# Performance work log

Measured on AMD Instinct MI355X. Metric: run time of the kernel, lower is better.

## Reference

```python
import jax, jax.numpy as jnp
import numpy as np

HQ, HK, DH = 32, 8, 64
ROPE_BASE = 10000.0


def _rope_tables(T, dtype):
    pos = jnp.arange(T, dtype=jnp.float32)
    inv_freq = 1.0 / (ROPE_BASE ** (jnp.arange(0, DH, 2, dtype=jnp.float32) / DH))
    freqs = pos[:, None] * inv_freq[None, :]          # (T, DH/2)
    cos = jnp.concatenate([jnp.cos(freqs), jnp.cos(freqs)], -1).astype(dtype)  # (T, DH)
    sin = jnp.concatenate([jnp.sin(freqs), jnp.sin(freqs)], -1).astype(dtype)
    return cos, sin


def _rotate_half(t):
    return jnp.concatenate([-t[..., DH // 2:], t[..., :DH // 2]], -1)


def setup_inputs() -> dict:
    key = jax.random.key(0)
    k1, k2, k3, k4 = jax.random.split(key, 4)
    B, T, D = 2, 2048, 2048
    std = 0.02 / np.sqrt(24)
    kv_std = std / np.sqrt(HQ / HK)
    return {
        "x": jax.random.normal(k1, (B, T, D), jnp.float32),
        "Wq": jax.random.normal(k2, (D, HQ * DH), jnp.float32) * std,
        "Wkv": jax.random.normal(k3, (D, 2 * HK * DH), jnp.float32) * kv_std,
        "Wo": jax.random.normal(k4, (HQ * DH, D), jnp.float32) * std,
    }


def reference(x, Wq, Wkv, Wo):
    B, T, D = x.shape
    g = HQ // HK
    scale = DH ** -0.5
    # projections
    q = (x @ Wq).reshape(B, T, HQ, DH).transpose(0, 2, 1, 3)       # (B,Hq,T,Dh)
    kv = (x @ Wkv).reshape(B, T, 2, HK, DH)
    k = kv[:, :, 0].transpose(0, 2, 1, 3)                           # (B,Hk,T,Dh)
    v = kv[:, :, 1].transpose(0, 2, 1, 3)
    # GQA expand: each kv head repeated g times consecutively
    k = jnp.repeat(k, g, axis=1)                                    # (B,Hq,T,Dh)
    v = jnp.repeat(v, g, axis=1)
    # RoPE on q and repeated k
    cos, sin = _rope_tables(T, x.dtype)
    q = q * cos + _rotate_half(q) * sin
    k = k * cos + _rotate_half(k) * sin
    # attention
    scores = jnp.einsum('bhqd,bhkd->bhqk', q, k) * scale            # (B,Hq,T,T)
    causal = jnp.triu(jnp.ones((T, T), bool), 1)
    scores = jnp.where(causal, -jnp.inf, scores)
    attn = jax.nn.softmax(scores.astype(jnp.float32), axis=-1).astype(x.dtype)
    out = jnp.einsum('bhqk,bhkd->bhqd', attn, v)                    # (B,Hq,T,Dh)
    out = out.transpose(0, 2, 1, 3).reshape(B, T, HQ * DH)
    return out @ Wo
```

## Files before the change

### kernel.cpp

```cpp
#include <hip/hip_runtime.h>
#include <hip/hip_bf16.h>

#define DEVI __device__ __forceinline__

typedef __attribute__((ext_vector_type(4))) float f32x4;
typedef __attribute__((ext_vector_type(16))) float f32x16;
typedef __attribute__((ext_vector_type(8))) short s16x8;
typedef __attribute__((ext_vector_type(4))) short s16x4;

DEVI ushort f2bf(float f) {
  union { float f; unsigned u; } v; v.f = f;
  unsigned r = v.u + 0x7FFFu + ((v.u >> 16) & 1u);
  return (ushort)(r >> 16);
}

DEVI void gload_lds16(const void* g, void* l) {
  __builtin_amdgcn_global_load_lds((const __attribute__((address_space(1))) void*)g,
                                   (__attribute__((address_space(3))) void*)l, 16, 0, 0);
}

template <int NITER>
DEVI void stage_swz(const ushort* __restrict__ gsrc, int stride_elems, ushort* lds, int tid) {
  const int wv = tid >> 6, ln = tid & 63;
  #pragma unroll
  for (int j = 0; j < NITER; ++j) {
    const int ci = j * 256 + wv * 64 + ln;
    const int row = ci >> 3, c = ci & 7;
    const ushort* src = gsrc + (size_t)row * stride_elems + ((c ^ (row & 7)) << 3);
    gload_lds16(src, lds + (size_t)(j * 256 + wv * 64) * 8);
  }
}

DEVI s16x8 frag_swz(const ushort* lds_tile, int row, int chunk) {
  const int off = row * 128 + ((chunk ^ (row & 7)) << 4);
  return *(const s16x8*)((const char*)lds_tile + off);
}

__global__ __launch_bounds__(256) void cast_bf16_k(const float* __restrict__ in,
                                                   ushort* __restrict__ out, int n) {
  int i = (blockIdx.x * 256 + threadIdx.x) * 4;
  if (i >= n) return;
  float4 v = *(const float4*)(in + i);
  ushort4 o;
  o.x = f2bf(v.x); o.y = f2bf(v.y); o.z = f2bf(v.z); o.w = f2bf(v.w);
  *(ushort4*)(out + i) = o;
}

__global__ __launch_bounds__(256) void transpose_cast_k(const float* __restrict__ in,
                                                        ushort* __restrict__ out, int R, int C) {
  __shared__ ushort tile[64][66];
  const int r0 = blockIdx.y * 64, c0 = blockIdx.x * 64;
  const int tid = threadIdx.x;
  #pragma unroll
  for (int j = 0; j < 16; ++j) {
    int idx = j * 256 + tid;
    int r = idx >> 6, c = idx & 63;
    tile[c][r] = f2bf(in[(size_t)(r0 + r) * C + c0 + c]);
  }
  __syncthreads();
  #pragma unroll
  for (int j = 0; j < 16; ++j) {
    int idx = j * 256 + tid;
    int c = idx >> 6, r = idx & 63;
    out[(size_t)(c0 + c) * R + r0 + r] = tile[c][r];
  }
}

__global__ __launch_bounds__(256) void rope_table_k(float2* __restrict__ tab) {
  int idx = blockIdx.x * 256 + threadIdx.x;
  int t = idx >> 5, i = idx & 31;
  float inv = expf(-(float)i * 0.28782313662425575f);
  float ang = (float)t * inv;
  tab[idx] = make_float2(cosf(ang), sinf(ang));
}

__global__ __launch_bounds__(256) void gemm_bt(const ushort* __restrict__ A,
                                               const ushort* __restrict__ BT,
                                               float* __restrict__ C, int M, int N, int K) {
  __shared__ __align__(128) ushort As[128 * 64];
  __shared__ __align__(128) ushort Bs[128 * 64];
  const int tid = threadIdx.x;
  const int ln = tid & 63, wv = tid >> 6;
  const int g = ln >> 4, l15 = ln & 15;
  const int wm = wv >> 1, wn = wv & 1;
  const int m0 = blockIdx.y * 128, n0 = blockIdx.x * 128;

  f32x4 zero = {0.f, 0.f, 0.f, 0.f};
  f32x4 acc[4][4];
  #pragma unroll
  for (int i = 0; i < 4; ++i)
    #pragma unroll
    for (int j = 0; j < 4; ++j) acc[i][j] = zero;

  for (int kt = 0; kt < K; kt += 64) {
    __syncthreads();
    stage_swz<4>(A + (size_t)m0 * K + kt, K, As, tid);
    stage_swz<4>(BT + (size_t)n0 * K + kt, K, Bs, tid);
    __syncthreads();
    #pragma unroll
    for (int ks = 0; ks < 2; ++ks) {
      s16x8 af[4], bfr[4];
      #pragma unroll
      for (int mi = 0; mi < 4; ++mi) af[mi] = frag_swz(As, wm * 64 + mi * 16 + l15, ks * 4 + g);
      #pragma unroll
      for (int ni = 0; ni < 4; ++ni) bfr[ni] = frag_swz(Bs, wn * 64 + ni * 16 + l15, ks * 4 + g);
      #pragma unroll
      for (int mi = 0; mi < 4; ++mi)
        #pragma unroll
        for (int ni = 0; ni < 4; ++ni)
          acc[mi][ni] = __builtin_amdgcn_mfma_f32_16x16x32_bf16(af[mi], bfr[ni], acc[mi][ni], 0, 0, 0);
    }
  }
  #pragma unroll
  for (int mi = 0; mi < 4; ++mi)
    #pragma unroll
    for (int r = 0; r < 4; ++r) {
      int row = m0 + wm * 64 + mi * 16 + g * 4 + r;
      float* crow = C + (size_t)row * N + n0 + wn * 64 + l15;
      #pragma unroll
      for (int ni = 0; ni < 4; ++ni) crow[ni * 16] = acc[mi][ni][r];
    }
}

__global__ __launch_bounds__(256) void gemm_qkv_fused(const ushort* __restrict__ A,
                                                      const ushort* __restrict__ BT,
                                                      const float2* __restrict__ tab,
                                                      ushort* __restrict__ Qp,
                                                      ushort* __restrict__ Kp,
                                                      ushort* __restrict__ Vp) {
  const int K = 2048;
  __shared__ __align__(128) ushort smem[128 * 132];
  ushort* As = smem;
  ushort* Bs = smem + 8192;
  ushort* Ot = smem;
  const int tid = threadIdx.x;
  const int ln = tid & 63, wv = tid >> 6;
  const int g = ln >> 4, l15 = ln & 15;
  const int l31 = ln & 31, hi = ln >> 5;
  const int wm = wv >> 1, wn = wv & 1;
  const int m0 = blockIdx.y * 128, n0 = blockIdx.x * 128;

  f32x4 zero = {0.f, 0.f, 0.f, 0.f};
  f32x4 acc[4][4];
  #pragma unroll
  for (int i = 0; i < 4; ++i)
    #pragma unroll
    for (int j = 0; j < 4; ++j) acc[i][j] = zero;

  for (int kt = 0; kt < K; kt += 64) {
    __syncthreads();
    stage_swz<4>(A + (size_t)m0 * K + kt, K, As, tid);
    stage_swz<4>(BT + (size_t)n0 * K + kt, K, Bs, tid);
    __syncthreads();
    #pragma unroll
    for (int ks = 0; ks < 2; ++ks) {
      s16x8 af[4], bfr[4];
      #pragma unroll
      for (int mi = 0; mi < 4; ++mi) af[mi] = frag_swz(As, wm * 64 + mi * 16 + l15, ks * 4 + g);
      #pragma unroll
      for (int ni = 0; ni < 4; ++ni) bfr[ni] = frag_swz(Bs, wn * 64 + ni * 16 + l15, ks * 4 + g);
      #pragma unroll
      for (int mi = 0; mi < 4; ++mi)
        #pragma unroll
        for (int ni = 0; ni < 4; ++ni)
          acc[mi][ni] = __builtin_amdgcn_mfma_f32_16x16x32_bf16(af[mi], bfr[ni], acc[mi][ni], 0, 0, 0);
    }
  }

  __syncthreads();
  const int bq = m0 >> 11;
  const int tg0 = m0 & 2047;
  const int type = (n0 < 2048) ? 0 : (n0 < 2560 ? 1 : 2);

  #pragma unroll
  for (int mi = 0; mi < 4; ++mi)
    #pragma unroll
    for (int r = 0; r < 4; ++r) {
      const int tl = wm * 64 + mi * 16 + g * 4 + r;
      const int t = tg0 + tl;
      #pragma unroll
      for (int ni = 0; ni < 4; ++ni) {
        const int cl = wn * 64 + ni * 16 + l15;
        float val = acc[mi][ni][r];
        float outv;
        if (type < 2) {
          float pairv = acc[mi][ni ^ 2][r];
          float2 cs = tab[t * 32 + (ni & 1) * 16 + l15];
          outv = (ni & 2) ? (val * cs.x + pairv * cs.y) : (val * cs.x - pairv * cs.y);
          if (type == 0) outv *= 0.18033688011112042f;
        } else {
          outv = val;
        }
        Ot[tl * 132 + cl] = f2bf(outv);
      }
    }
  __syncthreads();

  #pragma unroll
  for (int it = 0; it < 8; ++it) {
    const int id = wv * 8 + it;
    const int hl = id >> 4, q4 = (id >> 2) & 3, fi = id & 3;
    const int tile = (tg0 >> 5) + q4;
    if (type < 2) {
      const ushort* srow = Ot + (q4 * 32 + l31) * 132 + hl * 64 + fi * 16 + hi * 8;
      union { s16x4 h[2]; s16x8 v; } u;
      u.h[0] = *(const s16x4*)srow;
      u.h[1] = *(const s16x4*)(srow + 4);
      ushort* dst;
      if (type == 0) {
        const int h = (n0 >> 6) + hl;
        dst = Qp + (((size_t)(bq * 32 + h) * 64 + tile) * 4 + fi) * 512 + ln * 8;
      } else {
        const int h = ((n0 - 2048) >> 6) + hl;
        dst = Kp + (((size_t)(bq * 8 + h) * 64 + tile) * 4 + fi) * 512 + ln * 8;
      }
      *(s16x8*)dst = u.v;
    } else {
      const int hk = ((n0 - 2560) >> 6) + hl;
      const int col = hl * 64 + (fi & 1) * 32 + l31;
      const int row0 = q4 * 32 + (fi >> 1) * 16 + hi * 8;
      ushort o[8];
      #pragma unroll
      for (int j = 0; j < 8; ++j) o[j] = Ot[(row0 + j) * 132 + col];
      ushort* dst = Vp + (((size_t)(bq * 8 + hk) * 64 + tile) * 4 + fi) * 512 + ln * 8;
      *(s16x8*)dst = *(const s16x8*)o;
    }
  }
}

__global__ __launch_bounds__(256) void attn_k(const ushort* __restrict__ Qp,
                                              const ushort* __restrict__ Kp,
                                              const ushort* __restrict__ Vp,
                                              ushort* __restrict__ O) {
  __shared__ ushort ep[4][32 * 64];
  const int tid = threadIdx.x, wv = tid >> 6, ln = tid & 63;
  const int l31 = ln & 31, hi = ln >> 5;

  const int f = blockIdx.x + gridDim.x * (blockIdx.y + 32 * blockIdx.z);
  const int xcd = f & 7, j = f >> 3;
  const int pr = xcd + 8 * (j & 1);
  const int b = pr >> 3, hk = pr & 7;
  const int s = j >> 1;
  const int hq = hk * 4 + (s & 3);
  const int qtile = 63 - ((s >> 2) * 4 + wv);
  const int qw = qtile * 32;
  const int nt = qtile + 1;

  const ushort* Qh    = Qp + ((size_t)(b * 32 + hq)) * (64 * 2048);
  const ushort* Kbase = Kp + ((size_t)(b * 8 + hk)) * (64 * 2048);
  const ushort* Vbase = Vp + ((size_t)(b * 8 + hk)) * (64 * 2048);
  ushort* lds = ep[wv];

  s16x8 qf[4];
  {
    const ushort* qp_ = Qh + (size_t)qtile * 2048 + ln * 8;
    #pragma unroll
    for (int ks = 0; ks < 4; ++ks) qf[ks] = *(const s16x8*)(qp_ + ks * 512);
  }

  f32x16 oacc[2];
  #pragma unroll
  for (int dt = 0; dt < 2; ++dt)
    #pragma unroll
    for (int r = 0; r < 16; ++r) oacc[dt][r] = 0.f;
  float m = -1e30f, l = 0.f;

  const ushort* kp = Kbase + ln * 8;
  const ushort* vp = Vbase + ln * 8;

  s16x8 kf[4];
  #pragma unroll
  for (int ks = 0; ks < 4; ++ks) kf[ks] = *(const s16x8*)(kp + ks * 512);
  kp += 2048;

  s16x8 vc[4];
  union pfu { unsigned u[4]; s16x8 v; };
  pfu pf0, pf1;

  #pragma unroll 1
  for (int kt = 0; kt < nt; ++kt) {
    if (kt) {
      oacc[0] = __builtin_amdgcn_mfma_f32_32x32x16_bf16(vc[0], pf0.v, oacc[0], 0, 0, 0);
      oacc[1] = __builtin_amdgcn_mfma_f32_32x32x16_bf16(vc[1], pf0.v, oacc[1], 0, 0, 0);
      oacc[0] = __builtin_amdgcn_mfma_f32_32x32x16_bf16(vc[2], pf1.v, oacc[0], 0, 0, 0);
      oacc[1] = __builtin_amdgcn_mfma_f32_32x32x16_bf16(vc[3], pf1.v, oacc[1], 0, 0, 0);
    }
    #pragma unroll
    for (int fi2 = 0; fi2 < 4; ++fi2) vc[fi2] = *(const s16x8*)(vp + fi2 * 512);
    vp += 2048;

    f32x16 sp;
    #pragma unroll
    for (int r = 0; r < 16; ++r) sp[r] = 0.f;
    #pragma unroll
    for (int ks = 0; ks < 4; ++ks)
      sp = __builtin_amdgcn_mfma_f32_32x32x16_bf16(kf[ks], qf[ks], sp, 0, 0, 0);

    if (kt + 1 < nt) {
      #pragma unroll
      for (int ks = 0; ks < 4; ++ks) kf[ks] = *(const s16x8*)(kp + ks * 512);
      kp += 2048;
    }

    if (kt == qtile) {
      #pragma unroll
      for (int r = 0; r < 16; ++r) {
        int key = (r & 3) + 8 * (r >> 2) + 4 * hi;
        if (key > l31) sp[r] = -1e30f;
      }
    }

    float t0 = fmaxf(fmaxf(sp[0], sp[1]), sp[2]);
    float t1 = fmaxf(fmaxf(sp[3], sp[4]), sp[5]);
    float t2 = fmaxf(fmaxf(sp[6], sp[7]), sp[8]);
    float t3 = fmaxf(fmaxf(sp[9], sp[10]), sp[11]);
    float t4 = fmaxf(fmaxf(sp[12], sp[13]), sp[14]);
    float u0 = fmaxf(fmaxf(t0, t1), t2);
    float u1 = fmaxf(fmaxf(t3, t4), sp[15]);
    float pm = fmaxf(u0, u1);
    pm = fmaxf(pm, __shfl_xor(pm, 32, 64));

    if (__any(pm > m)) {
      float mn = fmaxf(m, pm);
      float alpha = __builtin_amdgcn_exp2f(m - mn);
      m = mn;
      l *= alpha;
      #pragma unroll
      for (int dt = 0; dt < 2; ++dt)
        #pragma unroll
        for (int r = 0; r < 16; ++r) oacc[dt][r] *= alpha;
    }

    #pragma unroll
    for (int r = 0; r < 16; ++r) sp[r] = __builtin_amdgcn_exp2f(sp[r] - m);
    {
      float a0 = sp[0] + sp[1], a1 = sp[2] + sp[3], a2 = sp[4] + sp[5], a3 = sp[6] + sp[7];
      float a4 = sp[8] + sp[9], a5 = sp[10] + sp[11], a6 = sp[12] + sp[13], a7 = sp[14] + sp[15];
      float b0 = a0 + a1, b1 = a2 + a3, b2 = a4 + a5, b3 = a6 + a7;
      float rs = (b0 + b1) + (b2 + b3);
      rs += __shfl_xor(rs, 32, 64);
      l += rs;
    }

    unsigned cw[8], xs[8];
    #pragma unroll
    for (int jj = 0; jj < 8; ++jj) {
      union { __hip_bfloat162 h; unsigned u; } pk;
      pk.h = __float22bfloat162_rn(make_float2(sp[2 * jj], sp[2 * jj + 1]));
      cw[jj] = pk.u;
    }
    #pragma unroll
    for (int jj = 0; jj < 8; ++jj) xs[jj] = __shfl_xor(cw[jj], 32, 64);
    pf0.u[0] = hi ? xs[2] : cw[0];
    pf0.u[1] = hi ? xs[3] : cw[1];
    pf0.u[2] = hi ? cw[2] : xs[0];
    pf0.u[3] = hi ? cw[3] : xs[1];
    pf1.u[0] = hi ? xs[6] : cw[4];
    pf1.u[1] = hi ? xs[7] : cw[5];
    pf1.u[2] = hi ? cw[6] : xs[4];
    pf1.u[3] = hi ? cw[7] : xs[5];
  }

  oacc[0] = __builtin_amdgcn_mfma_f32_32x32x16_bf16(vc[0], pf0.v, oacc[0], 0, 0, 0);
  oacc[1] = __builtin_amdgcn_mfma_f32_32x32x16_bf16(vc[1], pf0.v, oacc[1], 0, 0, 0);
  oacc[0] = __builtin_amdgcn_mfma_f32_32x32x16_bf16(vc[2], pf1.v, oacc[0], 0, 0, 0);
  oacc[1] = __builtin_amdgcn_mfma_f32_32x32x16_bf16(vc[3], pf1.v, oacc[1], 0, 0, 0);

  float invl = 1.0f / l;
  #pragma unroll
  for (int dt = 0; dt < 2; ++dt)
    #pragma unroll
    for (int r = 0; r < 16; ++r) {
      int d = dt * 32 + (r & 3) + 8 * (r >> 2) + 4 * hi;
      int byte = (l31 * 128 + d * 2) ^ ((l31 & 7) << 4);
      *(ushort*)((char*)lds + byte) = f2bf(oacc[dt][r] * invl);
    }
  const int qr = ln >> 1, half = ln & 1;
  #pragma unroll
  for (int jj = 0; jj < 4; ++jj) {
    int byte = (qr * 128 + half * 64 + jj * 16) ^ ((qr & 7) << 4);
    s16x8 vrow = *(const s16x8*)((const char*)lds + byte);
    *(s16x8*)(O + ((size_t)(b * 2048 + qw + qr)) * 2048 + hq * 64 + half * 32 + jj * 8) = vrow;
  }
}

extern "C" void kernel_launch(void* const* d_in, const int* in_sizes, int n_in,
                              void* d_out, int out_size, void* d_ws, size_t ws_size,
                              hipStream_t stream) {
  const float* x   = (const float*)d_in[0];
  const float* Wq  = (const float*)d_in[1];
  const float* Wkv = (const float*)d_in[2];
  const float* Wo  = (const float*)d_in[3];
  float* out = (float*)d_out;

  char* ws = (char*)d_ws;
  ushort* xb     = (ushort*)(ws);
  ushort* WqkvT  = (ushort*)(ws + 16777216);
  ushort* WoT    = (ushort*)(ws + 29360128);
  float2* tab    = (float2*)(ws + 37748736);
  ushort* Qp     = (ushort*)(ws + 38273024);
  ushort* Kp     = (ushort*)(ws + 55050240);
  ushort* Vp     = (ushort*)(ws + 59244544);
  ushort* Ob     = (ushort*)(ws + 63438848);

  cast_bf16_k<<<8192, 256, 0, stream>>>(x, xb, 2 * 2048 * 2048);
  transpose_cast_k<<<dim3(32, 32), 256, 0, stream>>>(Wq, WqkvT, 2048, 2048);
  transpose_cast_k<<<dim3(16, 32), 256, 0, stream>>>(Wkv, WqkvT + 2048 * 2048, 2048, 1024);
  transpose_cast_k<<<dim3(32, 32), 256, 0, stream>>>(Wo, WoT, 2048, 2048);
  rope_table_k<<<256, 256, 0, stream>>>(tab);
  gemm_qkv_fused<<<dim3(24, 32), 256, 0, stream>>>(xb, WqkvT, tab, Qp, Kp, Vp);
  attn_k<<<dim3(16, 32, 2), 256, 0, stream>>>(Qp, Kp, Vp, Ob);
  gemm_bt<<<dim3(16, 32), 256, 0, stream>>>(Ob, WoT, out, 4096, 2048, 2048);
}
```

Baseline: 247.5 us.

## Replace both GEMMs with a 256x256-tile double-buffered pipelined MFMA kernel

```diff
diff --git a/kernel.cpp b/kernel.cpp
--- a/kernel.cpp
+++ b/kernel.cpp
@@ -19,22 +19,8 @@
                                    (__attribute__((address_space(3))) void*)l, 16, 0, 0);
 }
 
-template <int NITER>
-DEVI void stage_swz(const ushort* __restrict__ gsrc, int stride_elems, ushort* lds, int tid) {
-  const int wv = tid >> 6, ln = tid & 63;
-  #pragma unroll
-  for (int j = 0; j < NITER; ++j) {
-    const int ci = j * 256 + wv * 64 + ln;
-    const int row = ci >> 3, c = ci & 7;
-    const ushort* src = gsrc + (size_t)row * stride_elems + ((c ^ (row & 7)) << 3);
-    gload_lds16(src, lds + (size_t)(j * 256 + wv * 64) * 8);
-  }
-}
-
-DEVI s16x8 frag_swz(const ushort* lds_tile, int row, int chunk) {
-  const int off = row * 128 + ((chunk ^ (row & 7)) << 4);
-  return *(const s16x8*)((const char*)lds_tile + off);
-}
+#define MFMA16 __builtin_amdgcn_mfma_f32_16x16x32_bf16
+#define SBAR() asm volatile("s_barrier" ::: "memory")
 
 __global__ __launch_bounds__(256) void cast_bf16_k(const float* __restrict__ in,
                                                    ushort* __restrict__ out, int n) {
@@ -74,156 +60,218 @@
   tab[idx] = make_float2(cosf(ang), sinf(ang));
 }
 
-__global__ __launch_bounds__(256) void gemm_bt(const ushort* __restrict__ A,
-                                               const ushort* __restrict__ BT,
-                                               float* __restrict__ C, int M, int N, int K) {
-  __shared__ __align__(128) ushort As[128 * 64];
-  __shared__ __align__(128) ushort Bs[128 * 64];
+template <int M, int N, int K, int EPI>
+__global__ __launch_bounds__(512, 2) void gemm256(const ushort* __restrict__ A,
+                                                  const ushort* __restrict__ BT,
+                                                  const float2* __restrict__ tab,
+                                                  float* __restrict__ C,
+                                                  ushort* __restrict__ Qp,
+                                                  ushort* __restrict__ Kp,
+                                                  ushort* __restrict__ Vp) {
+  constexpr int NKT = K / 64;
+  constexpr int GX = N / 256;
+  constexpr int NWG = (M / 256) * GX;
+  __shared__ __attribute__((aligned(128))) ushort smem[65536];
+
   const int tid = threadIdx.x;
   const int ln = tid & 63, wv = tid >> 6;
-  const int g = ln >> 4, l15 = ln & 15;
-  const int wm = wv >> 1, wn = wv & 1;
-  const int m0 = blockIdx.y * 128, n0 = blockIdx.x * 128;
-
-  f32x4 zero = {0.f, 0.f, 0.f, 0.f};
-  f32x4 acc[4][4];
-  #pragma unroll
-  for (int i = 0; i < 4; ++i)
-    #pragma unroll
-    for (int j = 0; j < 4; ++j) acc[i][j] = zero;
-
-  for (int kt = 0; kt < K; kt += 64) {
-    __syncthreads();
-    stage_swz<4>(A + (size_t)m0 * K + kt, K, As, tid);
-    stage_swz<4>(BT + (size_t)n0 * K + kt, K, Bs, tid);
-    __syncthreads();
+  const int g = ln >> 4, l15 = ln & 15, l31 = ln & 31, hi = ln >> 5;
+  const int wm = wv >> 2, wn = wv & 3;
+  const int wub = tid & ~63;
+
+  const int orig = blockIdx.x;
+  const int wg = (orig & 7) * (NWG / 8) + (orig >> 3);
+  const int bx = wg % GX, by = wg / GX;
+  const int m0 = by * 256, n0 = bx * 256;
+
+  ushort* Asm = smem;
+  ushort* Bsm = smem + 32768;
+
+  auto stageA = [&](int t, int h) {
+    const ushort* gs = A + (size_t)(m0 + h * 128) * K + t * 64;
+    ushort* ld = Asm + (t & 1) * 16384 + h * 8192;
+    #pragma unroll
+    for (int j = 0; j < 2; ++j) {
+      int ci = j * 512 + tid;
+      int row = ci >> 3, c = ci & 7;
+      gload_lds16(gs + (size_t)row * K + ((c ^ (row & 7)) << 3),
+                  ld + (size_t)(j * 512 + wub) * 8);
+    }
+  };
+  auto stageB = [&](int t, int h) {
+    const ushort* gs = BT + (size_t)(n0 + h * 128) * K + t * 64;
+    ushort* ld = Bsm + (t & 1) * 16384 + h * 8192;
+    #pragma unroll
+    for (int j = 0; j < 2; ++j) {
+      int ci = j * 512 + tid;
+      int row = ci >> 3, c = ci & 7;
+      gload_lds16(gs + (size_t)row * K + ((c ^ (row & 7)) << 3),
+                  ld + (size_t)(j * 512 + wub) * 8);
+    }
+  };
+  auto ldfrag = [&](const ushort* half, int row, int kc) -> s16x8 {
+    return *(const s16x8*)((const char*)half + row * 128 + ((kc ^ (row & 7)) << 4));
+  };
+
+  f32x4 acc[8][4];
+  #pragma unroll
+  for (int i = 0; i < 8; ++i)
+    #pragma unroll
+    for (int j = 0; j < 4; ++j) acc[i][j] = (f32x4){0.f, 0.f, 0.f, 0.f};
+
+  stageB(0, 0); stageB(0, 1); stageA(0, 0); stageA(0, 1);
+  stageB(1, 0); stageB(1, 1); stageA(1, 0);
+  asm volatile("s_waitcnt vmcnt(6)" ::: "memory");
+  SBAR();
+
+  #pragma unroll 1
+  for (int t = 0; t < NKT; ++t) {
+    const ushort* Ah = Asm + (t & 1) * 16384 + wm * 8192;
+    const ushort* Bh = Bsm + (t & 1) * 16384 + (wn >> 1) * 8192;
+    s16x8 a0[4][2], a1[4][2], bfr[4][2];
+
     #pragma unroll
     for (int ks = 0; ks < 2; ++ks) {
-      s16x8 af[4], bfr[4];
-      #pragma unroll
-      for (int mi = 0; mi < 4; ++mi) af[mi] = frag_swz(As, wm * 64 + mi * 16 + l15, ks * 4 + g);
-      #pragma unroll
-      for (int ni = 0; ni < 4; ++ni) bfr[ni] = frag_swz(Bs, wn * 64 + ni * 16 + l15, ks * 4 + g);
+      #pragma unroll
+      for (int ni = 0; ni < 4; ++ni)
+        bfr[ni][ks] = ldfrag(Bh, (wn & 1) * 64 + ni * 16 + l15, ks * 4 + g);
       #pragma unroll
       for (int mi = 0; mi < 4; ++mi)
-        #pragma unroll
-        for (int ni = 0; ni < 4; ++ni)
-          acc[mi][ni] = __builtin_amdgcn_mfma_f32_16x16x32_bf16(af[mi], bfr[ni], acc[mi][ni], 0, 0, 0);
-    }
-  }
-  #pragma unroll
-  for (int mi = 0; mi < 4; ++mi)
-    #pragma unroll
-    for (int r = 0; r < 4; ++r) {
-      int row = m0 + wm * 64 + mi * 16 + g * 4 + r;
-      float* crow = C + (size_t)row * N + n0 + wn * 64 + l15;
-      #pragma unroll
-      for (int ni = 0; ni < 4; ++ni) crow[ni * 16] = acc[mi][ni][r];
-    }
-}
-
-__global__ __launch_bounds__(256) void gemm_qkv_fused(const ushort* __restrict__ A,
-                                                      const ushort* __restrict__ BT,
-                                                      const float2* __restrict__ tab,
-                                                      ushort* __restrict__ Qp,
-                                                      ushort* __restrict__ Kp,
-                                                      ushort* __restrict__ Vp) {
-  const int K = 2048;
-  __shared__ __align__(128) ushort smem[128 * 132];
-  ushort* As = smem;
-  ushort* Bs = smem + 8192;
-  ushort* Ot = smem;
-  const int tid = threadIdx.x;
-  const int ln = tid & 63, wv = tid >> 6;
-  const int g = ln >> 4, l15 = ln & 15;
-  const int l31 = ln & 31, hi = ln >> 5;
-  const int wm = wv >> 1, wn = wv & 1;
-  const int m0 = blockIdx.y * 128, n0 = blockIdx.x * 128;
-
-  f32x4 zero = {0.f, 0.f, 0.f, 0.f};
-  f32x4 acc[4][4];
-  #pragma unroll
-  for (int i = 0; i < 4; ++i)
-    #pragma unroll
-    for (int j = 0; j < 4; ++j) acc[i][j] = zero;
-
-  for (int kt = 0; kt < K; kt += 64) {
-    __syncthreads();
-    stage_swz<4>(A + (size_t)m0 * K + kt, K, As, tid);
-    stage_swz<4>(BT + (size_t)n0 * K + kt, K, Bs, tid);
-    __syncthreads();
-    #pragma unroll
-    for (int ks = 0; ks < 2; ++ks) {
-      s16x8 af[4], bfr[4];
-      #pragma unroll
-      for (int mi = 0; mi < 4; ++mi) af[mi] = frag_swz(As, wm * 64 + mi * 16 + l15, ks * 4 + g);
-      #pragma unroll
-      for (int ni = 0; ni < 4; ++ni) bfr[ni] = frag_swz(Bs, wn * 64 + ni * 16 + l15, ks * 4 + g);
+        a0[mi][ks] = ldfrag(Ah, mi * 16 + l15, ks * 4 + g);
+    }
+    if (t + 1 < NKT) stageA(t + 1, 1);
+    SBAR();
+    __builtin_amdgcn_s_setprio(1);
+    #pragma unroll
+    for (int mi = 0; mi < 4; ++mi)
+      #pragma unroll
+      for (int ni = 0; ni < 2; ++ni)
+        #pragma unroll
+        for (int ks = 0; ks < 2; ++ks)
+          acc[mi][ni] = MFMA16(a0[mi][ks], bfr[ni][ks], acc[mi][ni], 0, 0, 0);
+    __builtin_amdgcn_s_setprio(0);
+    SBAR();
+
+    #pragma unroll
+    for (int ks = 0; ks < 2; ++ks)
       #pragma unroll
       for (int mi = 0; mi < 4; ++mi)
-        #pragma unroll
-        for (int ni = 0; ni < 4; ++ni)
-          acc[mi][ni] = __builtin_amdgcn_mfma_f32_16x16x32_bf16(af[mi], bfr[ni], acc[mi][ni], 0, 0, 0);
-    }
-  }
-
-  __syncthreads();
-  const int bq = m0 >> 11;
-  const int tg0 = m0 & 2047;
-  const int type = (n0 < 2048) ? 0 : (n0 < 2560 ? 1 : 2);
-
-  #pragma unroll
-  for (int mi = 0; mi < 4; ++mi)
-    #pragma unroll
-    for (int r = 0; r < 4; ++r) {
-      const int tl = wm * 64 + mi * 16 + g * 4 + r;
-      const int t = tg0 + tl;
-      #pragma unroll
-      for (int ni = 0; ni < 4; ++ni) {
-        const int cl = wn * 64 + ni * 16 + l15;
-        float val = acc[mi][ni][r];
-        float outv;
+        a1[mi][ks] = ldfrag(Ah, 64 + mi * 16 + l15, ks * 4 + g);
+    if (t + 2 < NKT) stageB(t + 2, 0);
+    SBAR();
+    __builtin_amdgcn_s_setprio(1);
+    #pragma unroll
+    for (int mi = 0; mi < 4; ++mi)
+      #pragma unroll
+      for (int ni = 0; ni < 2; ++ni)
+        #pragma unroll
+        for (int ks = 0; ks < 2; ++ks)
+          acc[mi][2 + ni] = MFMA16(a0[mi][ks], bfr[2 + ni][ks], acc[mi][2 + ni], 0, 0, 0);
+    __builtin_amdgcn_s_setprio(0);
+    SBAR();
+
+    if (t + 2 < NKT) stageB(t + 2, 1);
+    SBAR();
+    __builtin_amdgcn_s_setprio(1);
+    #pragma unroll
+    for (int mi = 0; mi < 4; ++mi)
+      #pragma unroll
+      for (int ni = 0; ni < 2; ++ni)
+        #pragma unroll
+        for (int ks = 0; ks < 2; ++ks)
+          acc[4 + mi][ni] = MFMA16(a1[mi][ks], bfr[ni][ks], acc[4 + mi][ni], 0, 0, 0);
+    __builtin_amdgcn_s_setprio(0);
+    SBAR();
+
+    if (t + 2 < NKT) stageA(t + 2, 0);
+    SBAR();
+    __builtin_amdgcn_s_setprio(1);
+    #pragma unroll
+    for (int mi = 0; mi < 4; ++mi)
+      #pragma unroll
+      for (int ni = 0; ni < 2; ++ni)
+        #pragma unroll
+        for (int ks = 0; ks < 2; ++ks)
+          acc[4 + mi][2 + ni] = MFMA16(a1[mi][ks], bfr[2 + ni][ks], acc[4 + mi][2 + ni], 0, 0, 0);
+    __builtin_amdgcn_s_setprio(0);
+    if (t + 2 < NKT)      asm volatile("s_waitcnt vmcnt(6)" ::: "memory");
+    else if (t + 1 < NKT) asm volatile("s_waitcnt vmcnt(0)" ::: "memory");
+    SBAR();
+  }
+
+  if constexpr (EPI == 0) {
+    #pragma unroll
+    for (int mi = 0; mi < 8; ++mi)
+      #pragma unroll
+      for (int r = 0; r < 4; ++r) {
+        int row = m0 + wm * 128 + mi * 16 + g * 4 + r;
+        float* crow = C + (size_t)row * N + n0 + wn * 64 + l15;
+        #pragma unroll
+        for (int ni = 0; ni < 4; ++ni) crow[ni * 16] = acc[mi][ni][r];
+      }
+  } else {
+    const int bq = by >> 3;
+    const int tb0 = (by & 7) * 256;
+    const int type = (bx < 8) ? 0 : (bx < 10 ? 1 : 2);
+    constexpr int OST = 260;
+
+    #pragma unroll 1
+    for (int hm = 0; hm < 2; ++hm) {
+      if (wm == hm) {
+        #pragma unroll
+        for (int mi = 0; mi < 8; ++mi)
+          #pragma unroll
+          for (int r = 0; r < 4; ++r) {
+            const int tl = mi * 16 + g * 4 + r;
+            const int t = tb0 + hm * 128 + tl;
+            #pragma unroll
+            for (int ni = 0; ni < 4; ++ni) {
+              const int cl = wn * 64 + ni * 16 + l15;
+              float val = acc[mi][ni][r], outv;
+              if (type < 2) {
+                float pairv = acc[mi][ni ^ 2][r];
+                float2 cs = tab[t * 32 + (ni & 1) * 16 + l15];
+                outv = (ni & 2) ? (val * cs.x + pairv * cs.y) : (val * cs.x - pairv * cs.y);
+                if (type == 0) outv *= 0.18033688011112042f;
+              } else {
+                outv = val;
+              }
+              smem[tl * OST + cl] = f2bf(outv);
+            }
+          }
+      }
+      SBAR();
+      #pragma unroll
+      for (int it = 0; it < 8; ++it) {
+        const int id = wv * 8 + it;
+        const int hl = id >> 4, q4 = (id >> 2) & 3, fi = id & 3;
+        const int tile = (by & 7) * 8 + hm * 4 + q4;
         if (type < 2) {
-          float pairv = acc[mi][ni ^ 2][r];
-          float2 cs = tab[t * 32 + (ni & 1) * 16 + l15];
-          outv = (ni & 2) ? (val * cs.x + pairv * cs.y) : (val * cs.x - pairv * cs.y);
-          if (type == 0) outv *= 0.18033688011112042f;
+          const ushort* srow = smem + (q4 * 32 + l31) * OST + hl * 64 + fi * 16 + hi * 8;
+          union { s16x4 h[2]; s16x8 v; } u;
+          u.h[0] = *(const s16x4*)srow;
+          u.h[1] = *(const s16x4*)(srow + 4);
+          ushort* dst;
+          if (type == 0) {
+            const int h = bx * 4 + hl;
+            dst = Qp + (((size_t)(bq * 32 + h) * 64 + tile) * 4 + fi) * 512 + ln * 8;
+          } else {
+            const int h = (bx - 8) * 4 + hl;
+            dst = Kp + (((size_t)(bq * 8 + h) * 64 + tile) * 4 + fi) * 512 + ln * 8;
+          }
+          *(s16x8*)dst = u.v;
         } else {
-          outv = val;
+          const int hk = (bx - 10) * 4 + hl;
+          const int col = hl * 64 + (fi & 1) * 32 + l31;
+          const int row0 = q4 * 32 + (fi >> 1) * 16 + hi * 8;
+          union { ushort o[8]; s16x8 v; } u;
+          #pragma unroll
+          for (int j2 = 0; j2 < 8; ++j2) u.o[j2] = smem[(row0 + j2) * OST + col];
+          ushort* dst = Vp + (((size_t)(bq * 8 + hk) * 64 + tile) * 4 + fi) * 512 + ln * 8;
+          *(s16x8*)dst = u.v;
         }
-        Ot[tl * 132 + cl] = f2bf(outv);
       }
-    }
-  __syncthreads();
-
-  #pragma unroll
-  for (int it = 0; it < 8; ++it) {
-    const int id = wv * 8 + it;
-    const int hl = id >> 4, q4 = (id >> 2) & 3, fi = id & 3;
-    const int tile = (tg0 >> 5) + q4;
-    if (type < 2) {
-      const ushort* srow = Ot + (q4 * 32 + l31) * 132 + hl * 64 + fi * 16 + hi * 8;
-      union { s16x4 h[2]; s16x8 v; } u;
-      u.h[0] = *(const s16x4*)srow;
-      u.h[1] = *(const s16x4*)(srow + 4);
-      ushort* dst;
-      if (type == 0) {
-        const int h = (n0 >> 6) + hl;
-        dst = Qp + (((size_t)(bq * 32 + h) * 64 + tile) * 4 + fi) * 512 + ln * 8;
-      } else {
-        const int h = ((n0 - 2048) >> 6) + hl;
-        dst = Kp + (((size_t)(bq * 8 + h) * 64 + tile) * 4 + fi) * 512 + ln * 8;
-      }
-      *(s16x8*)dst = u.v;
-    } else {
-      const int hk = ((n0 - 2560) >> 6) + hl;
-      const int col = hl * 64 + (fi & 1) * 32 + l31;
-      const int row0 = q4 * 32 + (fi >> 1) * 16 + hi * 8;
-      ushort o[8];
-      #pragma unroll
-      for (int j = 0; j < 8; ++j) o[j] = Ot[(row0 + j) * 132 + col];
-      ushort* dst = Vp + (((size_t)(bq * 8 + hk) * 64 + tile) * 4 + fi) * 512 + ln * 8;
-      *(s16x8*)dst = *(const s16x8*)o;
+      SBAR();
     }
   }
 }
@@ -408,7 +456,8 @@
   transpose_cast_k<<<dim3(16, 32), 256, 0, stream>>>(Wkv, WqkvT + 2048 * 2048, 2048, 1024);
   transpose_cast_k<<<dim3(32, 32), 256, 0, stream>>>(Wo, WoT, 2048, 2048);
   rope_table_k<<<256, 256, 0, stream>>>(tab);
-  gemm_qkv_fused<<<dim3(24, 32), 256, 0, stream>>>(xb, WqkvT, tab, Qp, Kp, Vp);
+  gemm256<4096, 3072, 2048, 1><<<192, 512, 0, stream>>>(xb, WqkvT, tab, (float*)nullptr, Qp, Kp, Vp);
   attn_k<<<dim3(16, 32, 2), 256, 0, stream>>>(Qp, Kp, Vp, Ob);
-  gemm_bt<<<dim3(16, 32), 256, 0, stream>>>(Ob, WoT, out, 4096, 2048, 2048);
-}
+  gemm256<4096, 2048, 2048, 0><<<128, 512, 0, stream>>>(Ob, WoT, (const float2*)nullptr, out,
+                                                        (ushort*)nullptr, (ushort*)nullptr, (ushort*)nullptr);
+}
```

After: 311.0 us. 25.7% more time.
